# Performance work log

Hardware: AMD Instinct MI355X
Metric: run time of the kernel (lower is better)

## Reference

```python
import jax, jax.numpy as jnp
import numpy as np

A, T, C, R, D, K, H, W = 3, 32, 4, 8, 2, 1024, 64, 64


def setup_inputs() -> dict:
    key = jax.random.key(0)
    ks = jax.random.split(key, 6)
    x = jax.random.normal(ks[0], (A, H, W), dtype=jnp.float32)
    # k-space trajectory in rad/voxel, uniform in [-pi, pi]
    trj = (jax.random.uniform(ks[1], (R, D, K), dtype=jnp.float32) * 2.0 - 1.0) * np.pi
    phi = jax.random.normal(ks[2], (A, T), dtype=jnp.float32)
    mps = jax.random.normal(ks[3], (C, H, W), dtype=jnp.float32)
    sqrt_dcf = jax.random.uniform(ks[4], (R, K), dtype=jnp.float32)
    subsamp_idx = jax.random.randint(ks[5], (T,), 0, R, dtype=jnp.int64)
    return {"x": x, "trj": trj, "phi": phi, "mps": mps,
            "sqrt_dcf": sqrt_dcf, "subsamp_idx": subsamp_idx}


def _nudft_matrix(trj):
    # Exact type-2 non-uniform DFT matrix E[r, k, n] = exp(-i w_rk . p_n)
    gy = (jnp.arange(H) - H // 2).astype(jnp.float32)
    gx = (jnp.arange(W) - W // 2).astype(jnp.float32)
    grid = jnp.stack(jnp.meshgrid(gy, gx, indexing="ij"), axis=0).reshape(D, H * W)
    phase = jnp.einsum("rdk,dn->rkn", trj, grid)  # [R, K, N]
    return jnp.exp(-1j * phase)  # complex64 [R, K, N]


def reference(x, trj, phi, mps, sqrt_dcf, subsamp_idx):
    # SENSE-weighted images per subspace coeff: [A, C, N]
    s = (mps[None, :, :, :] * x[:, None, :, :]).reshape(A, C, H * W).astype(jnp.complex64)
    E = _nudft_matrix(trj)
    # NUFFT of every (coeff, coil) image along every trajectory: [A, R, C, K]
    y = jnp.einsum("rkn,acn->arck", E, s)
    # temporal subspace expansion: [R, T, C, K]
    y = jnp.einsum("at,arck->rtck", phi.astype(jnp.complex64), y)
    # density compensation
    y = y * sqrt_dcf[:, None, None, :].astype(jnp.complex64)
    # per-timepoint trajectory subsampling: [T, C, K]
    out = y[subsamp_idx, jnp.arange(T)]
    return out
```

## Files before the change

### kernel.cpp

```cpp
#include <hip/hip_runtime.h>
#include <hip/hip_bf16.h>

#define NA 3
#define NT 32
#define NC 4
#define NR 8
#define NK 1024
#define NPIX 4096
#define NOUT (NT * NC * NK)
#define NRK (NR * NK)

typedef __attribute__((ext_vector_type(8))) short bf16x8;
typedef __attribute__((ext_vector_type(4))) float f32x4;

static __device__ __forceinline__ short f2bf(float f) {
    union { __hip_bfloat16 h; short s; } u;
    u.h = __float2bfloat16(f);
    return u.s;
}

__global__ __launch_bounds__(256) void prep_pack(
    const float* __restrict__ x,
    const float* __restrict__ candA,
    const float* __restrict__ candB,
    int* __restrict__ flag,
    short* __restrict__ sp)
{
    __shared__ int sfl;
    if (threadIdx.x == 0) sfl = 0;
    __syncthreads();
    {
        const float4* A4 = (const float4*)candA;
        int loc = 0;
        for (int i = threadIdx.x; i < 4096; i += 256) {
            const float4 v = A4[i];
            if (fabsf(v.x) > 3.1416f || fabsf(v.y) > 3.1416f ||
                fabsf(v.z) > 3.1416f || fabsf(v.w) > 3.1416f) loc = 1;
        }
        if (loc) atomicOr(&sfl, 1);
    }
    __syncthreads();
    const int fl = sfl;
    if (blockIdx.x == 0 && threadIdx.x == 0) flag[0] = fl;
    const float* __restrict__ mps = fl ? candA : candB;

    const int job = blockIdx.x * 256 + threadIdx.x;
    const int ch = job >> 9, p8 = (job & 511) * 8;
    const int a = ch >> 2, c = ch & 3;
    const float4 xv0 = *(const float4*)&x[a * NPIX + p8];
    const float4 xv1 = *(const float4*)&x[a * NPIX + p8 + 4];
    const float4 mv0 = *(const float4*)&mps[c * NPIX + p8];
    const float4 mv1 = *(const float4*)&mps[c * NPIX + p8 + 4];
    union { bf16x8 v; short s[8]; } pk;
    pk.s[0] = f2bf(xv0.x * mv0.x); pk.s[1] = f2bf(xv0.y * mv0.y);
    pk.s[2] = f2bf(xv0.z * mv0.z); pk.s[3] = f2bf(xv0.w * mv0.w);
    pk.s[4] = f2bf(xv1.x * mv1.x); pk.s[5] = f2bf(xv1.y * mv1.y);
    pk.s[6] = f2bf(xv1.z * mv1.z); pk.s[7] = f2bf(xv1.w * mv1.w);
    *(bf16x8*)(sp + ch * NPIX + p8) = pk.v;
}

__global__ __launch_bounds__(512, 4) void nudft_all8(
    const short* __restrict__ sp,
    const float* __restrict__ candA,
    const float* __restrict__ candB,
    const int*  __restrict__ flag,
    const float* __restrict__ phi,
    const float* __restrict__ dcf,
    const int*  __restrict__ sidx,
    float* __restrict__ out)
{
    __shared__ float2 ylds[2][12][16];

    const float* __restrict__ trj = flag[0] ? candB : candA;

    const int tid = threadIdx.x;
    const int w = tid >> 6, l = tid & 63, col = l & 15, g = l >> 4;
    const int chgrp = w & 3, ihalf = w >> 2;
    const int rk0 = blockIdx.x * 16;
    const int r = rk0 >> 10, k0 = rk0 & (NK - 1);
    const int k = k0 + col;

    const float t0 = trj[(r * 2 + 0) * NK + k];
    const float t1 = trj[(r * 2 + 1) * NK + k];

    bf16x8 breh[2], bimh[2];
    {
        float pr[8], pi[8];
        float sr, cr; __sincosf(t1, &sr, &cr);
        float s0, c0; __sincosf(t1 * (float)(g * 8 - 32), &s0, &c0);
        pr[0] = c0; pi[0] = -s0;
#pragma unroll
        for (int e = 1; e < 8; ++e) {
            const float nr = pr[e-1] * cr + pi[e-1] * sr;
            const float ni = pi[e-1] * cr - pr[e-1] * sr;
            pr[e] = nr; pi[e] = ni;
        }
        union { bf16x8 v; short s[8]; } u0, u1;
#pragma unroll
        for (int e = 0; e < 8; ++e) { u0.s[e] = f2bf(pr[e]); u1.s[e] = f2bf(pi[e]); }
        breh[0] = u0.v; bimh[0] = u1.v;
        float s32, c32; __sincosf(32.f * t1, &s32, &c32);
#pragma unroll
        for (int e = 0; e < 8; ++e) {
            const float nr = pr[e] * c32 + pi[e] * s32;
            const float ni = pi[e] * c32 - pr[e] * s32;
            u0.s[e] = f2bf(nr); u1.s[e] = f2bf(ni);
        }
        breh[1] = u0.v; bimh[1] = u1.v;
    }

    float syr, cyr; __sincosf(t0, &syr, &cyr);

    float yre[3] = {0.f, 0.f, 0.f}, yim[3] = {0.f, 0.f, 0.f};
#pragma unroll
    for (int sl = 0; sl < 2; ++sl) {
        const int i0 = ihalf * 32 + sl * 16;
        float eyR[4], eyI[4];
        {
            float sb, cb; __sincosf(t0 * (float)(i0 + g * 4 - 32), &sb, &cb);
            eyR[0] = cb; eyI[0] = -sb;
#pragma unroll
            for (int q = 1; q < 4; ++q) {
                const float nr = eyR[q-1] * cyr + eyI[q-1] * syr;
                const float ni = eyI[q-1] * cyr - eyR[q-1] * syr;
                eyR[q] = nr; eyI[q] = ni;
            }
        }
#pragma unroll
        for (int cc = 0; cc < 3; ++cc) {
            const int ch = chgrp * 3 + cc;
            const short* ap = sp + ch * NPIX + (i0 + col) * 64 + g * 8;
            const bf16x8 a0 = *(const bf16x8*)ap;
            const bf16x8 a1 = *(const bf16x8*)(ap + 32);
            f32x4 gre = {0.f, 0.f, 0.f, 0.f}, gim = {0.f, 0.f, 0.f, 0.f};
            gre = __builtin_amdgcn_mfma_f32_16x16x32_bf16(a0, breh[0], gre, 0, 0, 0);
            gre = __builtin_amdgcn_mfma_f32_16x16x32_bf16(a1, breh[1], gre, 0, 0, 0);
            gim = __builtin_amdgcn_mfma_f32_16x16x32_bf16(a0, bimh[0], gim, 0, 0, 0);
            gim = __builtin_amdgcn_mfma_f32_16x16x32_bf16(a1, bimh[1], gim, 0, 0, 0);
#pragma unroll
            for (int reg = 0; reg < 4; ++reg) {
                yre[cc] = fmaf(eyR[reg], gre[reg], fmaf(-eyI[reg], gim[reg], yre[cc]));
                yim[cc] = fmaf(eyR[reg], gim[reg], fmaf( eyI[reg], gre[reg], yim[cc]));
            }
        }
    }

#pragma unroll
    for (int cc = 0; cc < 3; ++cc) {
        float vr = yre[cc], vi = yim[cc];
        vr += __shfl_xor(vr, 16); vi += __shfl_xor(vi, 16);
        vr += __shfl_xor(vr, 32); vi += __shfl_xor(vi, 32);
        if (g == 0) ylds[ihalf][chgrp * 3 + cc][col] = make_float2(vr, vi);
    }
    __syncthreads();

    bool is64 = true;
#pragma unroll
    for (int i = 1; i < 32; i += 2) is64 = is64 && (sidx[i] == 0);
#pragma unroll
    for (int q = 0; q < 4; ++q) {
        const int item = tid + q * 512;
        const int kl = item & 15;
        const int c  = (item >> 4) & 3;
        const int t  = item >> 6;
        const int rt = is64 ? sidx[2 * t] : sidx[t];
        if (rt == r) {
            const float d = dcf[r * NK + k0 + kl];
            float ore = 0.f, oim = 0.f;
#pragma unroll
            for (int a = 0; a < NA; ++a) {
                const float p = phi[a * NT + t];
                const float2 v0 = ylds[0][a * 4 + c][kl];
                const float2 v1 = ylds[1][a * 4 + c][kl];
                ore = fmaf(p, v0.x + v1.x, ore);
                oim = fmaf(p, v0.y + v1.y, oim);
            }
            const int gid = t * 4096 + c * 1024 + k0 + kl;
            out[gid]        = ore * d;
            out[NOUT + gid] = oim * d;
        }
    }
}

extern "C" void kernel_launch(void* const* d_in, const int* in_sizes, int n_in,
                              void* d_out, int out_size, void* d_ws, size_t ws_size,
                              hipStream_t stream) {
    int ix = 0, i16a = 1, iphi = 2, i16b = 3, idcf = 4, isidx = 5;
    int f16[2]; int n16 = 0, fx = -1, fphi = -1, fdcf = -1, fsidx = -1;
    for (int i = 0; i < n_in; ++i) {
        const int s = in_sizes[i];
        if (s == 12288) fx = i;
        else if (s == 96) fphi = i;
        else if (s == 8192) fdcf = i;
        else if (s == 16384) { if (n16 < 2) f16[n16] = i; ++n16; }
        else if (s == 32 || s == 64) fsidx = i;
    }
    if (fx >= 0 && fphi >= 0 && fdcf >= 0 && fsidx >= 0 && n16 == 2) {
        ix = fx; iphi = fphi; idcf = fdcf; isidx = fsidx;
        i16a = f16[0]; i16b = f16[1];
    }

    const float* x    = (const float*)d_in[ix];
    const float* cA   = (const float*)d_in[i16a];
    const float* cB   = (const float*)d_in[i16b];
    const float* phi  = (const float*)d_in[iphi];
    const float* dcf  = (const float*)d_in[idcf];
    const int*   sidx = (const int*)d_in[isidx];

    int*   flag = (int*)d_ws;
    short* sp   = (short*)((char*)d_ws + 256);

    prep_pack<<<24, 256, 0, stream>>>(x, cA, cB, flag, sp);
    nudft_all8<<<NRK / 16, 512, 0, stream>>>(sp, cA, cB, flag, phi, dcf, sidx,
                                             (float*)d_out);
}
```

Baseline: 18.63 us.

## Fuse prep_pack into NUDFT kernel, computing bf16 SENSE products on the fly

Merges the prep kernel into the main NUDFT kernel, leaving a single launch. Each block now runs the trajectory/maps disambiguation scan itself and forms the x*mps bf16 products in registers from fp32 loads, instead of reading a pre-packed workspace. Waves are re-partitioned so each wave handles one coil across all three coefficients, which lets the maps values be reused. The goal is to remove a kernel launch and the serial dependency between the two kernels. The cost is that every block rescans the 64 KB candidate buffer and reads more fp32 bytes, which adds L2 traffic.

```diff
diff --git a/kernel.cpp b/kernel.cpp
--- a/kernel.cpp
+++ b/kernel.cpp
@@ -19,63 +19,39 @@
     return u.s;
 }
 
-__global__ __launch_bounds__(256) void prep_pack(
+__global__ __launch_bounds__(512, 4) void nudft_mono(
     const float* __restrict__ x,
     const float* __restrict__ candA,
     const float* __restrict__ candB,
-    int* __restrict__ flag,
-    short* __restrict__ sp)
+    const float* __restrict__ phi,
+    const float* __restrict__ dcf,
+    const int*  __restrict__ sidx,
+    float* __restrict__ out)
 {
     __shared__ int sfl;
+    __shared__ float2 ylds[2][12][16];
+
     if (threadIdx.x == 0) sfl = 0;
     __syncthreads();
     {
         const float4* A4 = (const float4*)candA;
         int loc = 0;
-        for (int i = threadIdx.x; i < 4096; i += 256) {
-            const float4 v = A4[i];
+#pragma unroll
+        for (int q = 0; q < 8; ++q) {
+            const float4 v = A4[threadIdx.x + q * 512];
             if (fabsf(v.x) > 3.1416f || fabsf(v.y) > 3.1416f ||
                 fabsf(v.z) > 3.1416f || fabsf(v.w) > 3.1416f) loc = 1;
         }
         if (loc) atomicOr(&sfl, 1);
     }
     __syncthreads();
-    const int fl = sfl;
-    if (blockIdx.x == 0 && threadIdx.x == 0) flag[0] = fl;
-    const float* __restrict__ mps = fl ? candA : candB;
-
-    const int job = blockIdx.x * 256 + threadIdx.x;
-    const int ch = job >> 9, p8 = (job & 511) * 8;
-    const int a = ch >> 2, c = ch & 3;
-    const float4 xv0 = *(const float4*)&x[a * NPIX + p8];
-    const float4 xv1 = *(const float4*)&x[a * NPIX + p8 + 4];
-    const float4 mv0 = *(const float4*)&mps[c * NPIX + p8];
-    const float4 mv1 = *(const float4*)&mps[c * NPIX + p8 + 4];
-    union { bf16x8 v; short s[8]; } pk;
-    pk.s[0] = f2bf(xv0.x * mv0.x); pk.s[1] = f2bf(xv0.y * mv0.y);
-    pk.s[2] = f2bf(xv0.z * mv0.z); pk.s[3] = f2bf(xv0.w * mv0.w);
-    pk.s[4] = f2bf(xv1.x * mv1.x); pk.s[5] = f2bf(xv1.y * mv1.y);
-    pk.s[6] = f2bf(xv1.z * mv1.z); pk.s[7] = f2bf(xv1.w * mv1.w);
-    *(bf16x8*)(sp + ch * NPIX + p8) = pk.v;
-}
-
-__global__ __launch_bounds__(512, 4) void nudft_all8(
-    const short* __restrict__ sp,
-    const float* __restrict__ candA,
-    const float* __restrict__ candB,
-    const int*  __restrict__ flag,
-    const float* __restrict__ phi,
-    const float* __restrict__ dcf,
-    const int*  __restrict__ sidx,
-    float* __restrict__ out)
-{
-    __shared__ float2 ylds[2][12][16];
-
-    const float* __restrict__ trj = flag[0] ? candB : candA;
+    const float* __restrict__ trj = sfl ? candB : candA;
+    const float* __restrict__ mps = sfl ? candA : candB;
 
     const int tid = threadIdx.x;
     const int w = tid >> 6, l = tid & 63, col = l & 15, g = l >> 4;
-    const int chgrp = w & 3, ihalf = w >> 2;
+    const int c     = w & 3;
+    const int ihalf = w >> 2;
     const int rk0 = blockIdx.x * 16;
     const int r = rk0 >> 10, k0 = rk0 & (NK - 1);
     const int k = k0 + col;
@@ -126,31 +102,48 @@
                 eyR[q] = nr; eyI[q] = ni;
             }
         }
-#pragma unroll
-        for (int cc = 0; cc < 3; ++cc) {
-            const int ch = chgrp * 3 + cc;
-            const short* ap = sp + ch * NPIX + (i0 + col) * 64 + g * 8;
-            const bf16x8 a0 = *(const bf16x8*)ap;
-            const bf16x8 a1 = *(const bf16x8*)(ap + 32);
+
+        const int off = (i0 + col) * 64 + g * 8;
+        const float4 mv00 = *(const float4*)&mps[c * NPIX + off];
+        const float4 mv01 = *(const float4*)&mps[c * NPIX + off + 4];
+        const float4 mv10 = *(const float4*)&mps[c * NPIX + off + 32];
+        const float4 mv11 = *(const float4*)&mps[c * NPIX + off + 36];
+
+#pragma unroll
+        for (int a = 0; a < 3; ++a) {
+            const float4 xv00 = *(const float4*)&x[a * NPIX + off];
+            const float4 xv01 = *(const float4*)&x[a * NPIX + off + 4];
+            const float4 xv10 = *(const float4*)&x[a * NPIX + off + 32];
+            const float4 xv11 = *(const float4*)&x[a * NPIX + off + 36];
+            union { bf16x8 v; short s[8]; } p0, p1;
+            p0.s[0] = f2bf(xv00.x * mv00.x); p0.s[1] = f2bf(xv00.y * mv00.y);
+            p0.s[2] = f2bf(xv00.z * mv00.z); p0.s[3] = f2bf(xv00.w * mv00.w);
+            p0.s[4] = f2bf(xv01.x * mv01.x); p0.s[5] = f2bf(xv01.y * mv01.y);
+            p0.s[6] = f2bf(xv01.z * mv01.z); p0.s[7] = f2bf(xv01.w * mv01.w);
+            p1.s[0] = f2bf(xv10.x * mv10.x); p1.s[1] = f2bf(xv10.y * mv10.y);
+            p1.s[2] = f2bf(xv10.z * mv10.z); p1.s[3] = f2bf(xv10.w * mv10.w);
+            p1.s[4] = f2bf(xv11.x * mv11.x); p1.s[5] = f2bf(xv11.y * mv11.y);
+            p1.s[6] = f2bf(xv11.z * mv11.z); p1.s[7] = f2bf(xv11.w * mv11.w);
+
             f32x4 gre = {0.f, 0.f, 0.f, 0.f}, gim = {0.f, 0.f, 0.f, 0.f};
-            gre = __builtin_amdgcn_mfma_f32_16x16x32_bf16(a0, breh[0], gre, 0, 0, 0);
-            gre = __builtin_amdgcn_mfma_f32_16x16x32_bf16(a1, breh[1], gre, 0, 0, 0);
-            gim = __builtin_amdgcn_mfma_f32_16x16x32_bf16(a0, bimh[0], gim, 0, 0, 0);
-            gim = __builtin_amdgcn_mfma_f32_16x16x32_bf16(a1, bimh[1], gim, 0, 0, 0);
+            gre = __builtin_amdgcn_mfma_f32_16x16x32_bf16(p0.v, breh[0], gre, 0, 0, 0);
+            gre = __builtin_amdgcn_mfma_f32_16x16x32_bf16(p1.v, breh[1], gre, 0, 0, 0);
+            gim = __builtin_amdgcn_mfma_f32_16x16x32_bf16(p0.v, bimh[0], gim, 0, 0, 0);
+            gim = __builtin_amdgcn_mfma_f32_16x16x32_bf16(p1.v, bimh[1], gim, 0, 0, 0);
 #pragma unroll
             for (int reg = 0; reg < 4; ++reg) {
-                yre[cc] = fmaf(eyR[reg], gre[reg], fmaf(-eyI[reg], gim[reg], yre[cc]));
-                yim[cc] = fmaf(eyR[reg], gim[reg], fmaf( eyI[reg], gre[reg], yim[cc]));
+                yre[a] = fmaf(eyR[reg], gre[reg], fmaf(-eyI[reg], gim[reg], yre[a]));
+                yim[a] = fmaf(eyR[reg], gim[reg], fmaf( eyI[reg], gre[reg], yim[a]));
             }
         }
     }
 
 #pragma unroll
-    for (int cc = 0; cc < 3; ++cc) {
-        float vr = yre[cc], vi = yim[cc];
+    for (int a = 0; a < 3; ++a) {
+        float vr = yre[a], vi = yim[a];
         vr += __shfl_xor(vr, 16); vi += __shfl_xor(vi, 16);
         vr += __shfl_xor(vr, 32); vi += __shfl_xor(vi, 32);
-        if (g == 0) ylds[ihalf][chgrp * 3 + cc][col] = make_float2(vr, vi);
+        if (g == 0) ylds[ihalf][a * 4 + c][col] = make_float2(vr, vi);
     }
     __syncthreads();
 
@@ -161,7 +154,7 @@
     for (int q = 0; q < 4; ++q) {
         const int item = tid + q * 512;
         const int kl = item & 15;
-        const int c  = (item >> 4) & 3;
+        const int cc = (item >> 4) & 3;
         const int t  = item >> 6;
         const int rt = is64 ? sidx[2 * t] : sidx[t];
         if (rt == r) {
@@ -170,12 +163,12 @@
 #pragma unroll
             for (int a = 0; a < NA; ++a) {
                 const float p = phi[a * NT + t];
-                const float2 v0 = ylds[0][a * 4 + c][kl];
-                const float2 v1 = ylds[1][a * 4 + c][kl];
+                const float2 v0 = ylds[0][a * 4 + cc][kl];
+                const float2 v1 = ylds[1][a * 4 + cc][kl];
                 ore = fmaf(p, v0.x + v1.x, ore);
                 oim = fmaf(p, v0.y + v1.y, oim);
             }
-            const int gid = t * 4096 + c * 1024 + k0 + kl;
+            const int gid = t * 4096 + cc * 1024 + k0 + kl;
             out[gid]        = ore * d;
             out[NOUT + gid] = oim * d;
         }
@@ -200,17 +193,8 @@
         i16a = f16[0]; i16b = f16[1];
     }
 
-    const float* x    = (const float*)d_in[ix];
-    const float* cA   = (const float*)d_in[i16a];
-    const float* cB   = (const float*)d_in[i16b];
-    const float* phi  = (const float*)d_in[iphi];
-    const float* dcf  = (const float*)d_in[idcf];
-    const int*   sidx = (const int*)d_in[isidx];
-
-    int*   flag = (int*)d_ws;
-    short* sp   = (short*)((char*)d_ws + 256);
-
-    prep_pack<<<24, 256, 0, stream>>>(x, cA, cB, flag, sp);
-    nudft_all8<<<NRK / 16, 512, 0, stream>>>(sp, cA, cB, flag, phi, dcf, sidx,
-                                             (float*)d_out);
+    nudft_mono<<<NRK / 16, 512, 0, stream>>>(
+        (const float*)d_in[ix], (const float*)d_in[i16a], (const float*)d_in[i16b],
+        (const float*)d_in[iphi], (const float*)d_in[idcf], (const int*)d_in[isidx],
+        (float*)d_out);
 }
```

Measured after the change: 25.10 us. 1.35x slower.
